# Optimization experiments

Hardware: AMD Instinct MI355X
Metric: run time of the kernel (lower is better)

The kernel has to match this reference:

```python
import jax, jax.numpy as jnp
import numpy as np

N, F, E = 2048, 4, 65536
D, H, FF = 256, 4, 2048  # d_model, n_heads, transformer feedforward dim
HD = D // H


def setup_inputs() -> dict:
    key = jax.random.key(0)
    ks = jax.random.split(key, 26)
    p = lambda k, shape, fan_in: (jax.random.normal(k, shape, jnp.float32) / np.sqrt(fan_in))
    return {
        "features": jax.random.normal(ks[0], (N, F), jnp.float32),
        "edges": jax.random.randint(ks[1], (2, E), 0, N, jnp.int64),
        # Embedder.linear: Linear(1, 256)
        "lin_w": p(ks[2], (D, 1), 1), "lin_b": jnp.zeros((D,), jnp.float32),
        # TransformerEncoderLayer self-attention
        "in_proj_w": p(ks[3], (3 * D, D), D), "in_proj_b": jnp.zeros((3 * D,), jnp.float32),
        "out_w": p(ks[4], (D, D), D), "out_b": jnp.zeros((D,), jnp.float32),
        "ln1_g": jnp.ones((D,), jnp.float32), "ln1_b": jnp.zeros((D,), jnp.float32),
        # feedforward
        "ffn_w1": p(ks[5], (FF, D), D), "ffn_b1": jnp.zeros((FF,), jnp.float32),
        "ffn_w2": p(ks[6], (D, FF), FF), "ffn_b2": jnp.zeros((D,), jnp.float32),
        "ln2_g": jnp.ones((D,), jnp.float32), "ln2_b": jnp.zeros((D,), jnp.float32),
        # 4 GCNConv layers (torch Linear convention: weight [out, in])
        "W1": p(ks[7], (512, D), D), "b1": jnp.zeros((512,), jnp.float32),
        "W2": p(ks[8], (512, 512), 512), "b2": jnp.zeros((512,), jnp.float32),
        "W3": p(ks[9], (512, 512), 512), "b3": jnp.zeros((512,), jnp.float32),
        "W4": p(ks[10], (512, 512), 512), "b4": jnp.zeros((512,), jnp.float32),
    }


def _layer_norm(x, g, b, eps=1e-5):
    m = jnp.mean(x, axis=-1, keepdims=True)
    v = jnp.mean((x - m) ** 2, axis=-1, keepdims=True)
    return (x - m) / jnp.sqrt(v + eps) * g + b


def _gcn_conv(x, W, b, src, dst, n):
    # PyG GCNConv: h = x @ W^T; add self-loops; norm = deg^-1/2[src]*deg^-1/2[dst];
    # out = scatter_add(norm * h[src] -> dst) + bias
    h = x @ W.T
    loop = jnp.arange(n, dtype=src.dtype)
    s = jnp.concatenate([src, loop])
    d = jnp.concatenate([dst, loop])
    deg = jax.ops.segment_sum(jnp.ones_like(d, dtype=h.dtype), d, num_segments=n)
    dinv = jnp.where(deg > 0, deg ** -0.5, 0.0)
    norm = dinv[s] * dinv[d]
    return jax.ops.segment_sum(h[s] * norm[:, None], d, num_segments=n) + b


def reference(features, edges, lin_w, lin_b, in_proj_w, in_proj_b, out_w, out_b,
              ln1_g, ln1_b, ffn_w1, ffn_b1, ffn_w2, ffn_b2, ln2_g, ln2_b,
              W1, b1, W2, b2, W3, b3, W4, b4):
    n, f = features.shape
    # Embedder: [N,F,1] -> Linear(1,D) -> [N,F,D]; seq-first transformer (seq=N, batch=F)
    x = features[..., None] @ lin_w.T + lin_b  # [N,F,D]
    qkv = x @ in_proj_w.T + in_proj_b          # [N,F,3D]
    q, k, v = jnp.split(qkv, 3, axis=-1)
    split = lambda t: t.reshape(n, f, H, HD).transpose(1, 2, 0, 3)  # [F,H,N,hd]
    q, k, v = split(q), split(k), split(v)
    scores = jnp.einsum('bhqd,bhkd->bhqk', q, k) / np.sqrt(HD)      # [F,H,N,N]
    attn = jax.nn.softmax(scores, axis=-1)
    o = jnp.einsum('bhqk,bhkd->bhqd', attn, v).transpose(2, 0, 1, 3).reshape(n, f, D)
    o = o @ out_w.T + out_b
    x = _layer_norm(x + o, ln1_g, ln1_b)
    ff = jax.nn.relu(x @ ffn_w1.T + ffn_b1) @ ffn_w2.T + ffn_b2
    x = _layer_norm(x + ff, ln2_g, ln2_b)
    x = jax.nn.relu(jnp.mean(x, axis=1))  # mean over feature-batch dim -> [N,D]

    src, dst = edges[0], edges[1]
    x = jax.nn.relu(_gcn_conv(x, W1, b1, src, dst, n))
    x = jax.nn.relu(_gcn_conv(x, W2, b2, src, dst, n))
    x = jax.nn.relu(_gcn_conv(x, W3, b3, src, dst, n))
    x = _gcn_conv(x, W4, b4, src, dst, n)
    return x
```

## Files before the change

### kernel.cpp

```cpp
#include <hip/hip_runtime.h>
#include <hip/hip_bf16.h>
#include <math.h>

#define NN   2048
#define FB   4
#define DD   256
#define EE   65536
#define NT   (NN*FB)
#define FFD  2048

typedef unsigned int u32;
typedef unsigned short u16;
typedef __attribute__((ext_vector_type(4))) float f32x4;
typedef __attribute__((ext_vector_type(8))) short bf16x8;

#define OFF_W2   0
#define OFF_G1   524288
#define OFF_G2   655360
#define OFF_G3   917504
#define OFF_G4   1179648
#define WBF_TOT  1441792

__device__ float g_A[768], g_B[768];
__device__ float g_coefA[4], g_coefC[4];
__device__ float g_meanv[6], g_G[36];
__device__ float g_Vx[8*DD];
__device__ u16   g_w1vh[FFD*8];
__device__ float g_m[NT*4];
__device__ float g_cc[NT*8];
__device__ u16   g_xmh[NN*DD];
__device__ u16   g_hsh[NN*512];
__device__ u16   g_xgh[NN*512];
__device__ u16   g_wbf[WBF_TOT];
__device__ __align__(64) int g_degp[NN*16];
__device__ __align__(64) int g_curp[NN*16];
__device__ int   g_off[NN+1], g_adj[EE];
__device__ float g_dinv[NN];

__device__ __forceinline__ u16 f2bf(float x) {
  u32 u = __float_as_uint(x);
  return (u16)((u + 0x7FFFu + ((u >> 16) & 1u)) >> 16);
}
__device__ __forceinline__ float bfl(u32 v) { return __uint_as_float(v << 16); }
__device__ __forceinline__ float bfh(u32 v) { return __uint_as_float(v & 0xffff0000u); }
__device__ __forceinline__ void gl_lds16(const void* g, void* l) {
  __builtin_amdgcn_global_load_lds(
      (const __attribute__((address_space(1))) u32*)g,
      (__attribute__((address_space(3))) u32*)l, 16, 0, 0);
}
__device__ __forceinline__ float qred(float v) {
  v += __shfl_xor(v, 1, 64);
  v += __shfl_xor(v, 2, 64);
  return v;
}
__device__ __forceinline__ void acc8(const uint4 v, float* a) {
  a[0]+=bfl(v.x); a[1]+=bfh(v.x);
  a[2]+=bfl(v.y); a[3]+=bfh(v.y);
  a[4]+=bfl(v.z); a[5]+=bfh(v.z);
  a[6]+=bfl(v.w); a[7]+=bfh(v.w);
}

__global__ __launch_bounds__(256) void k_fuse1(const float* __restrict__ ipw,
    const float* __restrict__ ipb, const float* __restrict__ linw,
    const float* __restrict__ linb) {
  __shared__ __align__(16) float sm[512];
  const int b = blockIdx.x, t = threadIdx.x;
  if (b < 12) {
    float* lw = sm; float* lb = sm + 256;
    lw[t] = linw[t]; lb[t] = linb[t];
    __syncthreads();
    int j = b*64 + (t>>2), c = t&3;
    const float4* row = (const float4*)&ipw[j*256 + c*64];
    float a = 0.f, bb = 0.f;
    #pragma unroll
    for (int q = 0; q < 16; q++) {
      float4 v = row[q]; int d0 = c*64 + q*4;
      a  += v.x*lw[d0] + v.y*lw[d0+1] + v.z*lw[d0+2] + v.w*lw[d0+3];
      bb += v.x*lb[d0] + v.y*lb[d0+1] + v.z*lb[d0+2] + v.w*lb[d0+3];
    }
    a = qred(a); bb = qred(bb);
    if (c == 0) { g_A[j] = a; g_B[j] = bb + ipb[j]; }
  } else {
    int i = (b - 12)*256 + t;
    if (i < NN*16) { g_degp[i] = 0; g_curp[i] = 0; }
  }
}

__global__ __launch_bounds__(256) void k_fuse2(const float* __restrict__ outw,
    const float* __restrict__ outb, const float* __restrict__ linw,
    const float* __restrict__ linb, const float* __restrict__ g1,
    const float* __restrict__ b1ln, const int* __restrict__ edges) {
  __shared__ __align__(16) float sm[512 + 4*27];
  const int b = blockIdx.x, t = threadIdx.x;
  if (b == 0) {
    int lane = t & 63, w = t >> 6;
    {
      float aq = g_A[w*64 + lane], ak = g_A[256 + w*64 + lane], bq = g_B[w*64 + lane];
      float pa = aq * ak, pc = bq * ak;
      #pragma unroll
      for (int o = 32; o > 0; o >>= 1) { pa += __shfl_down(pa, o, 64); pc += __shfl_down(pc, o, 64); }
      if (lane == 0) { g_coefA[w] = pa * 0.125f; g_coefC[w] = pc * 0.125f; }
    }
    float* A2 = sm; float* B2 = sm + 256; float* wred = sm + 512;
    A2[t] = g_A[512 + t]; B2[t] = g_B[512 + t];
    __syncthreads();
    const int d = t;
    const float4* row = (const float4*)&outw[d*256];
    float pv[4] = {0,0,0,0}, q0 = 0.f;
    #pragma unroll 8
    for (int q = 0; q < 64; q++) {
      float4 v = row[q]; int e0 = q*4; int h = q >> 4;
      pv[h] += v.x*A2[e0] + v.y*A2[e0+1] + v.z*A2[e0+2] + v.w*A2[e0+3];
      q0    += v.x*B2[e0] + v.y*B2[e0+1] + v.z*B2[e0+2] + v.w*B2[e0+3];
    }
    q0 += outb[d];
    float c0 = linb[d] + q0;
    float Mv[6] = { linw[d], pv[0], pv[1], pv[2], pv[3], c0 };
    float vals[27];
    { int idx = 0;
      #pragma unroll
      for (int k = 0; k < 6; k++) vals[idx++] = Mv[k];
      #pragma unroll
      for (int k = 0; k < 6; k++)
        #pragma unroll
        for (int l = 0; l < 6; l++) if (l >= k) vals[idx++] = Mv[k]*Mv[l];
    }
    #pragma unroll
    for (int k2 = 0; k2 < 27; k2++) {
      float v = vals[k2];
      #pragma unroll
      for (int o = 32; o > 0; o >>= 1) v += __shfl_down(v, o, 64);
      if (lane == 0) wred[w*27 + k2] = v;
    }
    __syncthreads();
    if (t < 27) {
      float s = wred[t] + wred[27 + t] + wred[54 + t] + wred[81 + t];
      if (t < 6) g_meanv[t] = s * (1.f/256.f);
      else {
        int p = t - 6, k = 0;
        while (p >= 6 - k) { p -= 6 - k; k++; }
        int l = k + p;
        g_G[k*6+l] = s; g_G[l*6+k] = s;
      }
    }
    #pragma unroll
    for (int k = 0; k < 6; k++) g_Vx[k*256 + d] = Mv[k] * g1[d];
    g_Vx[6*256 + d] = g1[d];
    g_Vx[7*256 + d] = b1ln[d];
  } else {
    int e = (b - 1)*256 + t;
    atomicAdd(&g_degp[edges[EE + e] * 16], 1);
  }
}

__global__ __launch_bounds__(256) void k_fuse3(const float* __restrict__ feat,
    const float* __restrict__ w1, const float* __restrict__ fb1,
    const float* __restrict__ w2c, const float* __restrict__ W1c,
    const float* __restrict__ W2c, const float* __restrict__ W3c,
    const float* __restrict__ W4c) {
  __shared__ __align__(16) char smraw[34816];
  const int b = blockIdx.x, t = threadIdx.x;
  if (b < 512) {
    float* fs = (float*)smraw;
    float* ss = fs + 8192;
    float* ww = ss + 256;
    for (int i = t; i < 2048; i += 256) {
      const float4 v = *(const float4*)&feat[i*4];
      fs[0*2048+i] = v.x; fs[1*2048+i] = v.y; fs[2*2048+i] = v.z; fs[3*2048+i] = v.w;
    }
    __syncthreads();
    int tuple = b * 64 + (t >> 2);
    int c = t & 3;
    int h = tuple & 3, f = (tuple >> 2) & 3, n = tuple >> 4;
    float fi = fs[f*2048 + n];
    float tt = g_coefA[h] * fi + g_coefC[h];
    float s = 0.f, wsum = 0.f;
    int j0 = c * 512;
    for (int j = j0; j < j0 + 512; j++) {
      float fj = fs[f*2048 + j];
      float e = __expf(tt * fj);
      s += e; wsum += e * fj;
    }
    ss[(t>>2)*4 + c] = s; ww[(t>>2)*4 + c] = wsum;
    __syncthreads();
    if (c == 0) {
      float S = ss[(t>>2)*4] + ss[(t>>2)*4+1] + ss[(t>>2)*4+2] + ss[(t>>2)*4+3];
      float W = ww[(t>>2)*4] + ww[(t>>2)*4+1] + ww[(t>>2)*4+2] + ww[(t>>2)*4+3];
      g_m[tuple] = W / S;
    }
  } else if (b < 544) {
    float* vx = (float*)smraw;
    #pragma unroll
    for (int k = 0; k < 8; k++) vx[k*256 + t] = g_Vx[k*256 + t];
    __syncthreads();
    int j = (b - 512)*64 + (t>>2), c = t&3;
    const float4* row = (const float4*)&w1[j*256 + c*64];
    float acc[8] = {0,0,0,0,0,0,0,0};
    #pragma unroll
    for (int q = 0; q < 16; q++) {
      float4 v = row[q]; int d0 = c*64 + q*4;
      #pragma unroll
      for (int k = 0; k < 8; k++)
        acc[k] += v.x*vx[k*256+d0] + v.y*vx[k*256+d0+1]
                + v.z*vx[k*256+d0+2] + v.w*vx[k*256+d0+3];
    }
    #pragma unroll
    for (int k = 0; k < 8; k++) acc[k] = qred(acc[k]);
    if (c == 0) {
      acc[7] += fb1[j];
      uint4 r;
      r.x = ((u32)f2bf(acc[1])<<16) | f2bf(acc[0]);
      r.y = ((u32)f2bf(acc[3])<<16) | f2bf(acc[2]);
      r.z = ((u32)f2bf(acc[5])<<16) | f2bf(acc[4]);
      r.w = ((u32)f2bf(acc[7])<<16) | f2bf(acc[6]);
      *(uint4*)&g_w1vh[j*8] = r;
    }
  } else if (b == 544) {
    int* wt = (int*)smraw;
    int base = t * 8;
    int v[8], ex[8], sum = 0;
    #pragma unroll
    for (int i = 0; i < 8; i++) { ex[i] = sum; v[i] = g_degp[(base+i)*16]; sum += v[i]; }
    int lane = t & 63, w = t >> 6;
    int inc = sum;
    #pragma unroll
    for (int o = 1; o < 64; o <<= 1) { int x = __shfl_up(inc, o, 64); if (lane >= o) inc += x; }
    if (lane == 63) wt[w] = inc;
    __syncthreads();
    int wb = 0;
    for (int j = 0; j < w; j++) wb += wt[j];
    int excl = wb + inc - sum;
    #pragma unroll
    for (int i = 0; i < 8; i++) {
      g_off[base+i] = excl + ex[i];
      g_dinv[base+i] = rsqrtf((float)(v[i] + 1));
    }
    if (t == 255) g_off[NN] = wb + inc;
  } else {
    int i = ((b - 545)*256 + t) * 4;
    const float* src; int off;
    if (i < OFF_G1)      { src = w2c; off = OFF_W2; }
    else if (i < OFF_G2) { src = W1c; off = OFF_G1; }
    else if (i < OFF_G3) { src = W2c; off = OFF_G2; }
    else if (i < OFF_G4) { src = W3c; off = OFF_G3; }
    else                 { src = W4c; off = OFF_G4; }
    float4 v = *(const float4*)&src[i - off];
    ushort4 r;
    r.x = f2bf(v.x); r.y = f2bf(v.y); r.z = f2bf(v.z); r.w = f2bf(v.w);
    *(ushort4*)&g_wbf[i] = r;
  }
}

__global__ __launch_bounds__(256) void k_fuse4(const float* __restrict__ feat) {
  const int b = blockIdx.x, t = threadIdx.x;
  int tok = b * 256 + t;
  int n = tok >> 2, f = tok & 3;
  float fi = feat[n*4 + f];
  float u[6] = { fi, g_m[tok*4+0], g_m[tok*4+1], g_m[tok*4+2], g_m[tok*4+3], 1.f };
  float mu = 0.f;
  #pragma unroll
  for (int k = 0; k < 6; k++) mu += g_meanv[k] * u[k];
  float q = 0.f;
  for (int k = 0; k < 6; k++)
    for (int l = 0; l < 6; l++) q += u[k] * g_G[k*6+l] * u[l];
  q *= (1.f/256.f);
  float var = q - mu * mu;
  float s = rsqrtf(var + 1e-5f);
  float4 w0; w0.x = fi*s; w0.y = u[1]*s; w0.z = u[2]*s; w0.w = u[3]*s;
  float4 w1v; w1v.x = u[4]*s; w1v.y = s; w1v.z = -mu*s; w1v.w = 1.f;
  *(float4*)&g_cc[tok*8]     = w0;
  *(float4*)&g_cc[tok*8 + 4] = w1v;
}

__global__ __launch_bounds__(256) void k_ffnln(const float* __restrict__ fb2,
    const float* __restrict__ ln2g, const float* __restrict__ ln2b,
    const int* __restrict__ edges) {
  __shared__ __align__(16) char smp[149504];
  u16*   Bsl  = (u16*)smp;
  u16*   Asl  = (u16*)(smp + 131072);
  float* ccs  = (float*)(smp + 147456);
  float* part = (float*)(smp + 148480);

  const int b = blockIdx.x, t = threadIdx.x;
  if (b >= 256) {
    int e = (b - 256)*256 + t;
    int s = edges[e], d = edges[EE + e];
    int pos = atomicAdd(&g_curp[d*16], 1);
    g_adj[g_off[d] + pos] = s;
    return;
  }
  const int w = t >> 6, lane = t & 63, fr = lane & 15, gk = lane >> 4;
  const int tok0 = b * 32;
  const u16* W2p = g_wbf + OFF_W2;

  if (t < 64) ((float4*)ccs)[t] = ((const float4*)&g_cc[tok0*8])[t];
  __syncthreads();

  const int arow = t >> 3;
  const int sb = (t & 7) * 2;
  float ac[8];
  #pragma unroll
  for (int k = 0; k < 8; k++) ac[k] = ccs[arow*8 + k];

  f32x4 acc[2][4] = {};

  auto AGEN = [&](int it, int buf) {
    const int k0 = it << 7;
    #pragma unroll
    for (int sj = 0; sj < 2; sj++) {
      int s = sb + sj;
      float h[8];
      #pragma unroll
      for (int e2 = 0; e2 < 8; e2++) {
        uint4 wv = *(const uint4*)&g_w1vh[(size_t)(k0 + s*8 + e2)*8];
        float sv = ac[0]*bfl(wv.x) + ac[1]*bfh(wv.x)
                 + ac[2]*bfl(wv.y) + ac[3]*bfh(wv.y)
                 + ac[4]*bfl(wv.z) + ac[5]*bfh(wv.z)
                 + ac[6]*bfl(wv.w) + ac[7]*bfh(wv.w);
        h[e2] = fmaxf(sv, 0.f);
      }
      uint4 r;
      r.x = ((u32)f2bf(h[1])<<16) | f2bf(h[0]);
      r.y = ((u32)f2bf(h[3])<<16) | f2bf(h[2]);
      r.z = ((u32)f2bf(h[5])<<16) | f2bf(h[4]);
      r.w = ((u32)f2bf(h[7])<<16) | f2bf(h[6]);
      int ph = (s & 8) | ((s ^ (arow & 7)) & 7);
      *(uint4*)&Asl[(buf << 12) + (arow << 7) + (ph << 3)] = r;
    }
  };
  auto STAGE = [&](int it, int buf) {
    const int k0 = it << 7;
    #pragma unroll
    for (int c = 0; c < 16; c++) {
      int col0 = (w << 6) + (c << 2);
      int colL = col0 + (lane >> 4);
      int p = lane & 15;
      int q = (p & 8) | ((p ^ (colL & 7)) & 7);
      gl_lds16(W2p + (size_t)colL*FFD + k0 + q*8, Bsl + (buf << 15) + (col0 << 7));
    }
  };

  AGEN(0, 0);
  STAGE(0, 0);
  for (int it = 0; it < 16; ++it) {
    const int cur = it & 1;
    if (it < 15) {
      AGEN(it + 1, cur ^ 1);
      STAGE(it + 1, cur ^ 1);
    } else {
      asm volatile("s_waitcnt vmcnt(0)" ::: "memory");
    }
    asm volatile("s_waitcnt lgkmcnt(0)" ::: "memory");
    __builtin_amdgcn_sched_barrier(0);
    __builtin_amdgcn_s_barrier();
    __builtin_amdgcn_sched_barrier(0);
    #pragma unroll
    for (int kk = 0; kk < 4; kk++) {
      int qa = (kk << 2) + gk;
      #pragma unroll
      for (int rb = 0; rb < 2; rb++) {
        int row = rb*16 + fr;
        int pa = (qa & 8) | ((qa ^ (row & 7)) & 7);
        bf16x8 af = *(const bf16x8*)&Asl[(cur << 12) + (row << 7) + (pa << 3)];
        #pragma unroll
        for (int nb = 0; nb < 4; nb++) {
          int col = (w << 6) + (nb << 4) + fr;
          int pb = (qa & 8) | ((qa ^ (col & 7)) & 7);
          bf16x8 bv = *(const bf16x8*)&Bsl[(cur << 15) + (col << 7) + (pb << 3)];
          acc[rb][nb] = __builtin_amdgcn_mfma_f32_16x16x32_bf16(af, bv, acc[rb][nb], 0, 0, 0);
        }
      }
    }
    __builtin_amdgcn_sched_barrier(0);
    __builtin_amdgcn_s_barrier();
  }

  #pragma unroll
  for (int rb = 0; rb < 2; rb++)
    #pragma unroll
    for (int nb = 0; nb < 4; nb++) {
      int col = (w << 6) + (nb << 4) + fr;
      float fb = fb2[col];
      #pragma unroll
      for (int r = 0; r < 4; r++) {
        int row = rb*16 + gk*4 + r;
        float x1 = 0.f;
        #pragma unroll
        for (int k = 0; k < 8; k++) x1 += ccs[row*8 + k] * g_Vx[k*256 + col];
        acc[rb][nb][r] += fb + x1;
      }
    }
  float s1[2][4] = {}, s2v[2][4] = {};
  #pragma unroll
  for (int rb = 0; rb < 2; rb++)
    #pragma unroll
    for (int r = 0; r < 4; r++)
      #pragma unroll
      for (int nb = 0; nb < 4; nb++) {
        float v = acc[rb][nb][r];
        s1[rb][r] += v; s2v[rb][r] += v*v;
      }
  #pragma unroll
  for (int o = 1; o < 16; o <<= 1) {
    #pragma unroll
    for (int rb = 0; rb < 2; rb++)
      #pragma unroll
      for (int r = 0; r < 4; r++) {
        s1[rb][r]  += __shfl_xor(s1[rb][r],  o, 64);
        s2v[rb][r] += __shfl_xor(s2v[rb][r], o, 64);
      }
  }
  if (fr == 0) {
    #pragma unroll
    for (int rb = 0; rb < 2; rb++)
      #pragma unroll
      for (int r = 0; r < 4; r++) {
        int row = rb*16 + gk*4 + r;
        part[(w*32 + row)*2 + 0] = s1[rb][r];
        part[(w*32 + row)*2 + 1] = s2v[rb][r];
      }
  }
  __syncthreads();
  float mu[2][4], inv[2][4];
  #pragma unroll
  for (int rb = 0; rb < 2; rb++)
    #pragma unroll
    for (int r = 0; r < 4; r++) {
      int row = rb*16 + gk*4 + r;
      float S1 = 0.f, S2 = 0.f;
      #pragma unroll
      for (int wv = 0; wv < 4; wv++) {
        S1 += part[(wv*32 + row)*2 + 0];
        S2 += part[(wv*32 + row)*2 + 1];
      }
      float m = S1 * (1.f/256.f);
      mu[rb][r] = m;
      inv[rb][r] = rsqrtf(S2 * (1.f/256.f) - m*m + 1e-5f);
    }
  #pragma unroll
  for (int rb = 0; rb < 2; rb++) {
    int node = b*8 + rb*4 + gk;
    #pragma unroll
    for (int nb = 0; nb < 4; nb++) {
      int col = (w << 6) + (nb << 4) + fr;
      float g = ln2g[col], bb = ln2b[col];
      float m = 0.f;
      #pragma unroll
      for (int r = 0; r < 4; r++)
        m += (acc[rb][nb][r] - mu[rb][r]) * inv[rb][r] * g + bb;
      g_xmh[node*256 + col] = f2bf(fmaxf(m * 0.25f, 0.f));
    }
  }
}

template<int DO_ROWSCALE, int OUT_BF16, int HAS_BIAS>
__global__ __launch_bounds__(256) void k_mm64(
    const u16* __restrict__ A, const u16* __restrict__ Bm, void* __restrict__ Cv,
    int M, int N, int K,
    const float* __restrict__ rowscale, const float* __restrict__ bias)
{
  __shared__ u16 Asl[32*128];
  __shared__ u16 Bsl[64*128];
  const int t = threadIdx.x;
  const int w = t >> 6, lane = t & 63;
  const int bm = blockIdx.y * 32, bn = blockIdx.x * 64;
  const int wr = w >> 1, wc = w & 1;
  const int fr = lane & 15;
  const int gk = lane >> 4;
  f32x4 acc[2] = {};
  for (int k0 = 0; k0 < K; k0 += 128) {
    #pragma unroll
    for (int c = 0; c < 2; c++) {
      int row0 = (w << 3) + (c << 2);
      int rowL = row0 + (lane >> 4);
      int p = lane & 15;
      int q = (p & 8) | ((p ^ (rowL & 7)) & 7);
      gl_lds16(A + (size_t)(bm + rowL)*K + k0 + q*8, Asl + (row0 << 7));
    }
    #pragma unroll
    for (int c = 0; c < 4; c++) {
      int row0 = (w << 4) + (c << 2);
      int rowL = row0 + (lane >> 4);
      int p = lane & 15;
      int q = (p & 8) | ((p ^ (rowL & 7)) & 7);
      gl_lds16(Bm + (size_t)(bn + rowL)*K + k0 + q*8, Bsl + (row0 << 7));
    }
    __syncthreads();
    #pragma unroll
    for (int kk = 0; kk < 4; kk++) {
      int qa = (kk << 2) + gk;
      int row = wr*16 + fr;
      int pa = (qa & 8) | ((qa ^ (row & 7)) & 7);
      bf16x8 af = *(const bf16x8*)&Asl[(row << 7) + (pa << 3)];
      #pragma unroll
      for (int nb = 0; nb < 2; nb++) {
        int col = wc*32 + nb*16 + fr;
        int pb = (qa & 8) | ((qa ^ (col & 7)) & 7);
        bf16x8 bv = *(const bf16x8*)&Bsl[(col << 7) + (pb << 3)];
        acc[nb] = __builtin_amdgcn_mfma_f32_16x16x32_bf16(af, bv, acc[nb], 0, 0, 0);
      }
    }
    __syncthreads();
  }
  #pragma unroll
  for (int r = 0; r < 4; r++) {
    int row = bm + wr*16 + gk*4 + r;
    float rs = DO_ROWSCALE ? rowscale[row] : 1.f;
    #pragma unroll
    for (int nb = 0; nb < 2; nb++) {
      int col = bn + wc*32 + nb*16 + fr;
      float v = acc[nb][r];
      if (HAS_BIAS) v += bias[col];
      if (DO_ROWSCALE) v *= rs;
      if (OUT_BF16) ((u16*)Cv)[(size_t)row*N + col] = f2bf(v);
      else ((float*)Cv)[(size_t)row*N + col] = v;
    }
  }
}

template<int OUT_BF16, int DO_RELU>
__global__ __launch_bounds__(256) void k_agg(const float* __restrict__ bias,
                                             void* __restrict__ outv) {
  __shared__ __align__(16) float red[2][512];
  const int t = threadIdx.x, w = t >> 6, lane = t & 63;
  const int pair = w >> 1, half = w & 1;
  const int i = blockIdx.x*2 + pair;
  const int d = lane * 8;
  const uint4* tbl = (const uint4*)g_hsh;
  float a[8] = {0,0,0,0,0,0,0,0};
  int e0 = g_off[i], e1 = g_off[i+1];
  int mid = (e0 + e1) >> 1;
  int es = half ? mid : e0;
  int ee = half ? e1 : mid;
  if (!half) acc8(tbl[i*64 + lane], a);
  int e = es;
  for (; e + 4 <= ee; e += 4) {
    int s0 = g_adj[e+0], s1 = g_adj[e+1], s2 = g_adj[e+2], s3 = g_adj[e+3];
    uint4 v0 = tbl[s0*64 + lane];
    uint4 v1 = tbl[s1*64 + lane];
    uint4 v2 = tbl[s2*64 + lane];
    uint4 v3 = tbl[s3*64 + lane];
    acc8(v0, a); acc8(v1, a); acc8(v2, a); acc8(v3, a);
  }
  for (; e < ee; e++) acc8(tbl[g_adj[e]*64 + lane], a);
  if (!half) {
    #pragma unroll
    for (int q = 0; q < 8; q++) red[pair][d + q] = a[q];
  }
  __syncthreads();
  if (half) {
    #pragma unroll
    for (int q = 0; q < 8; q++) a[q] += red[pair][d + q];
    float di = g_dinv[i];
    const float4 b0 = *(const float4*)&bias[d];
    const float4 b1 = *(const float4*)&bias[d+4];
    a[0]=di*a[0]+b0.x; a[1]=di*a[1]+b0.y; a[2]=di*a[2]+b0.z; a[3]=di*a[3]+b0.w;
    a[4]=di*a[4]+b1.x; a[5]=di*a[5]+b1.y; a[6]=di*a[6]+b1.z; a[7]=di*a[7]+b1.w;
    if (DO_RELU) {
      #pragma unroll
      for (int q = 0; q < 8; q++) a[q] = fmaxf(a[q], 0.f);
    }
    if (OUT_BF16) {
      uint4 r;
      r.x = ((u32)f2bf(a[1])<<16) | f2bf(a[0]);
      r.y = ((u32)f2bf(a[3])<<16) | f2bf(a[2]);
      r.z = ((u32)f2bf(a[5])<<16) | f2bf(a[4]);
      r.w = ((u32)f2bf(a[7])<<16) | f2bf(a[6]);
      *(uint4*)&((u16*)outv)[i*512 + d] = r;
    } else {
      float4 r0; r0.x=a[0]; r0.y=a[1]; r0.z=a[2]; r0.w=a[3];
      float4 r1; r1.x=a[4]; r1.y=a[5]; r1.z=a[6]; r1.w=a[7];
      *(float4*)&((float*)outv)[i*512 + d]     = r0;
      *(float4*)&((float*)outv)[i*512 + d + 4] = r1;
    }
  }
}

static float* symf(const void* s) { void* p = nullptr; (void)hipGetSymbolAddress(&p, s); return (float*)p; }

extern "C" void kernel_launch(void* const* d_in, const int* in_sizes, int n_in,
                              void* d_out, int out_size, void* d_ws, size_t ws_size,
                              hipStream_t stream) {
  const float* feat = (const float*)d_in[0];
  const int*   edges= (const int*)  d_in[1];
  const float* linw = (const float*)d_in[2];
  const float* linb = (const float*)d_in[3];
  const float* ipw  = (const float*)d_in[4];
  const float* ipb  = (const float*)d_in[5];
  const float* outw = (const float*)d_in[6];
  const float* outb = (const float*)d_in[7];
  const float* ln1g = (const float*)d_in[8];
  const float* ln1b = (const float*)d_in[9];
  const float* fw1  = (const float*)d_in[10];
  const float* fb1  = (const float*)d_in[11];
  const float* fw2  = (const float*)d_in[12];
  const float* fb2  = (const float*)d_in[13];
  const float* ln2g = (const float*)d_in[14];
  const float* ln2b = (const float*)d_in[15];
  const float* W1g  = (const float*)d_in[16];
  const float* b1g  = (const float*)d_in[17];
  const float* W2g  = (const float*)d_in[18];
  const float* b2g  = (const float*)d_in[19];
  const float* W3g  = (const float*)d_in[20];
  const float* b3g  = (const float*)d_in[21];
  const float* W4g  = (const float*)d_in[22];
  const float* b4g  = (const float*)d_in[23];
  float* out = (float*)d_out;

  u16*   p_xmh = (u16*)symf(HIP_SYMBOL(g_xmh));
  u16*   p_hsh = (u16*)symf(HIP_SYMBOL(g_hsh));
  u16*   p_xgh = (u16*)symf(HIP_SYMBOL(g_xgh));
  u16*   p_wbf = (u16*)symf(HIP_SYMBOL(g_wbf));
  float* p_dinv= symf(HIP_SYMBOL(g_dinv));

  k_fuse1<<<140,  256, 0, stream>>>(ipw, ipb, linw, linb);
  k_fuse2<<<257,  256, 0, stream>>>(outw, outb, linw, linb, ln1g, ln1b, edges);
  k_fuse3<<<1953, 256, 0, stream>>>(feat, fw1, fb1, fw2, W1g, W2g, W3g, W4g);
  k_fuse4<<<32,   256, 0, stream>>>(feat);

  k_ffnln<<<512, 256, 0, stream>>>(fb2, ln2g, ln2b, edges);

  k_mm64<1,1,0><<<dim3(8, 64), 256, 0, stream>>>(
      p_xmh, p_wbf + OFF_G1, p_hsh, NN, 512, 256, p_dinv, nullptr);
  k_agg<1,1><<<NN/2, 256, 0, stream>>>(b1g, p_xgh);
  k_mm64<1,1,0><<<dim3(8, 64), 256, 0, stream>>>(
      p_xgh, p_wbf + OFF_G2, p_hsh, NN, 512, 512, p_dinv, nullptr);
  k_agg<1,1><<<NN/2, 256, 0, stream>>>(b2g, p_xgh);
  k_mm64<1,1,0><<<dim3(8, 64), 256, 0, stream>>>(
      p_xgh, p_wbf + OFF_G3, p_hsh, NN, 512, 512, p_dinv, nullptr);
  k_agg<1,1><<<NN/2, 256, 0, stream>>>(b3g, p_xgh);
  k_mm64<1,1,0><<<dim3(8, 64), 256, 0, stream>>>(
      p_xgh, p_wbf + OFF_G4, p_hsh, NN, 512, 512, p_dinv, nullptr);
  k_agg<0,0><<<NN/2, 256, 0, stream>>>(b4g, out);
}
```

Measured before the change: 178.0 us.

## Single-buffer W2 tiles and stage W1 slice in LDS to raise occupancy

The FFN kernel drops double buffering of the W2 and A tiles, cutting LDS from about 146KB to 78KB so two blocks can share a CU. The per-token W1 values are now loaded into a swizzled, double-buffered LDS slice by one wave instead of being read from global memory by every thread. In exchange, global loads for W2 no longer overlap the MFMA loop, and each iteration now has two full barriers, so latency hiding depends on the second resident block.

```diff
diff --git a/kernel.cpp b/kernel.cpp
--- a/kernel.cpp
+++ b/kernel.cpp
@@ -275,11 +275,12 @@
 __global__ __launch_bounds__(256) void k_ffnln(const float* __restrict__ fb2,
     const float* __restrict__ ln2g, const float* __restrict__ ln2b,
     const int* __restrict__ edges) {
-  __shared__ __align__(16) char smp[149504];
+  __shared__ __align__(16) char smp[79872];
   u16*   Bsl  = (u16*)smp;
-  u16*   Asl  = (u16*)(smp + 131072);
-  float* ccs  = (float*)(smp + 147456);
-  float* part = (float*)(smp + 148480);
+  u16*   Asl  = (u16*)(smp + 65536);
+  u16*   w1sl = (u16*)(smp + 73728);
+  float* ccs  = (float*)(smp + 77824);
+  float* part = (float*)(smp + 78848);
 
   const int b = blockIdx.x, t = threadIdx.x;
   if (b >= 256) {
@@ -294,6 +295,14 @@
   const u16* W2p = g_wbf + OFF_W2;
 
   if (t < 64) ((float4*)ccs)[t] = ((const float4*)&g_cc[tok0*8])[t];
+  if (w == 1) {
+    #pragma unroll
+    for (int hh = 0; hh < 2; hh++) {
+      int p = hh*64 + lane;
+      int q = (p & ~7) | ((p ^ (p >> 3)) & 7);
+      gl_lds16(g_w1vh + (size_t)q*8, w1sl + (hh << 9));
+    }
+  }
   __syncthreads();
 
   const int arow = t >> 3;
@@ -303,16 +312,33 @@
   for (int k = 0; k < 8; k++) ac[k] = ccs[arow*8 + k];
 
   f32x4 acc[2][4] = {};
-
-  auto AGEN = [&](int it, int buf) {
+  for (int it = 0; it < 16; it++) {
     const int k0 = it << 7;
+    const int cur = it & 1;
+    #pragma unroll
+    for (int c = 0; c < 16; c++) {
+      int col0 = (w << 6) + (c << 2);
+      int colL = col0 + (lane >> 4);
+      int p = lane & 15;
+      int q = (p & 8) | ((p ^ (colL & 7)) & 7);
+      gl_lds16(W2p + (size_t)colL*FFD + k0 + q*8, Bsl + (col0 << 7));
+    }
+    if (w == 1 && it < 15) {
+      #pragma unroll
+      for (int hh = 0; hh < 2; hh++) {
+        int p = hh*64 + lane;
+        int q = (p & ~7) | ((p ^ (p >> 3)) & 7);
+        gl_lds16(g_w1vh + (size_t)(k0 + 128 + q)*8, w1sl + ((cur ^ 1) << 10) + (hh << 9));
+      }
+    }
     #pragma unroll
     for (int sj = 0; sj < 2; sj++) {
       int s = sb + sj;
       float h[8];
       #pragma unroll
       for (int e2 = 0; e2 < 8; e2++) {
-        uint4 wv = *(const uint4*)&g_w1vh[(size_t)(k0 + s*8 + e2)*8];
+        int ph = s*8 + (e2 ^ (s & 7));
+        uint4 wv = *(const uint4*)&w1sl[(cur << 10) + ph*8];
         float sv = ac[0]*bfl(wv.x) + ac[1]*bfh(wv.x)
                  + ac[2]*bfl(wv.y) + ac[3]*bfh(wv.y)
                  + ac[4]*bfl(wv.z) + ac[5]*bfh(wv.z)
@@ -324,36 +350,10 @@
       r.y = ((u32)f2bf(h[3])<<16) | f2bf(h[2]);
       r.z = ((u32)f2bf(h[5])<<16) | f2bf(h[4]);
       r.w = ((u32)f2bf(h[7])<<16) | f2bf(h[6]);
-      int ph = (s & 8) | ((s ^ (arow & 7)) & 7);
-      *(uint4*)&Asl[(buf << 12) + (arow << 7) + (ph << 3)] = r;
-    }
-  };
-  auto STAGE = [&](int it, int buf) {
-    const int k0 = it << 7;
-    #pragma unroll
-    for (int c = 0; c < 16; c++) {
-      int col0 = (w << 6) + (c << 2);
-      int colL = col0 + (lane >> 4);
-      int p = lane & 15;
-      int q = (p & 8) | ((p ^ (colL & 7)) & 7);
-      gl_lds16(W2p + (size_t)colL*FFD + k0 + q*8, Bsl + (buf << 15) + (col0 << 7));
-    }
-  };
-
-  AGEN(0, 0);
-  STAGE(0, 0);
-  for (int it = 0; it < 16; ++it) {
-    const int cur = it & 1;
-    if (it < 15) {
-      AGEN(it + 1, cur ^ 1);
-      STAGE(it + 1, cur ^ 1);
-    } else {
-      asm volatile("s_waitcnt vmcnt(0)" ::: "memory");
-    }
-    asm volatile("s_waitcnt lgkmcnt(0)" ::: "memory");
-    __builtin_amdgcn_sched_barrier(0);
-    __builtin_amdgcn_s_barrier();
-    __builtin_amdgcn_sched_barrier(0);
+      int ph2 = (s & 8) | ((s ^ (arow & 7)) & 7);
+      *(uint4*)&Asl[(arow << 7) + (ph2 << 3)] = r;
+    }
+    __syncthreads();
     #pragma unroll
     for (int kk = 0; kk < 4; kk++) {
       int qa = (kk << 2) + gk;
@@ -361,18 +361,17 @@
       for (int rb = 0; rb < 2; rb++) {
         int row = rb*16 + fr;
         int pa = (qa & 8) | ((qa ^ (row & 7)) & 7);
-        bf16x8 af = *(const bf16x8*)&Asl[(cur << 12) + (row << 7) + (pa << 3)];
+        bf16x8 af = *(const bf16x8*)&Asl[(row << 7) + (pa << 3)];
         #pragma unroll
         for (int nb = 0; nb < 4; nb++) {
           int col = (w << 6) + (nb << 4) + fr;
           int pb = (qa & 8) | ((qa ^ (col & 7)) & 7);
-          bf16x8 bv = *(const bf16x8*)&Bsl[(cur << 15) + (col << 7) + (pb << 3)];
+          bf16x8 bv = *(const bf16x8*)&Bsl[(col << 7) + (pb << 3)];
           acc[rb][nb] = __builtin_amdgcn_mfma_f32_16x16x32_bf16(af, bv, acc[rb][nb], 0, 0, 0);
         }
       }
     }
-    __builtin_amdgcn_sched_barrier(0);
-    __builtin_amdgcn_s_barrier();
+    __syncthreads();
   }
 
   #pragma unroll
```

After: 170.5 us. 4.2% less time.
